# Kernel optimization log

Measured on AMD Instinct MI355X. Metric: run time of the kernel, lower is better.

## Reference

```python
import jax, jax.numpy as jnp
import numpy as np

EMBED_DIM = 1024
BLOCK = 2048
HEAD = 64
BATCH = 4


def setup_inputs() -> dict:
    key = jax.random.key(0)
    k0, k1, k2, k3 = jax.random.split(key, 4)
    tokens = jax.random.normal(k0, (BATCH, BLOCK, EMBED_DIM), dtype=jnp.float32)
    # torch Linear(embed_dim, head_size, bias=False): init ~ U(-1/sqrt(in), 1/sqrt(in)).
    s = 1.0 / np.sqrt(EMBED_DIM)
    Wq = jax.random.uniform(k1, (EMBED_DIM, HEAD), jnp.float32, -s, s)
    Wk = jax.random.uniform(k2, (EMBED_DIM, HEAD), jnp.float32, -s, s)
    Wv = jax.random.uniform(k3, (EMBED_DIM, HEAD), jnp.float32, -s, s)
    return {"tokens": tokens, "Wq": Wq, "Wk": Wk, "Wv": Wv}


def reference(tokens, Wq, Wk, Wv):
    B, S, E = tokens.shape
    q = jnp.einsum('bse,eh->bsh', tokens, Wq)
    k = jnp.einsum('bse,eh->bsh', tokens, Wk)
    v = jnp.einsum('bse,eh->bsh', tokens, Wv)
    # NOTE: module scales by embed_dim**-0.5 (not head_size).
    wei = jnp.einsum('bqh,bkh->bqk', q, k) * (E ** -0.5)
    causal = jnp.tril(jnp.ones((S, S), dtype=bool))  # tril_mask[:block,:block]
    wei = jnp.where(causal, wei, -1e9)
    wei = jax.nn.softmax(wei, axis=-1)
    # dropout(p=0.3) is identity in eval mode (deterministic reference)
    return jnp.einsum('bqk,bkh->bqh', wei, v)
```

## Files before the change

kernel.cpp:

```cpp
#include <hip/hip_runtime.h>
#include <stdint.h>


typedef __bf16 bf16_t;
typedef __bf16 bf16x8 __attribute__((ext_vector_type(8)));
typedef __bf16 bf16x4 __attribute__((ext_vector_type(4)));
typedef float floatx4 __attribute__((ext_vector_type(4)));

#define MFMA16(a, b, c) __builtin_amdgcn_mfma_f32_16x16x32_bf16((a), (b), (c), 0, 0, 0)

static constexpr float kQScale = 0.04508422002778f;
#define NEG_BIG (-3.0e38f)

__device__ inline bf16x4 cvt4(float4 f) {
  bf16x4 v;
  v[0] = (bf16_t)f.x; v[1] = (bf16_t)f.y; v[2] = (bf16_t)f.z; v[3] = (bf16_t)f.w;
  return v;
}

__global__ __launch_bounds__(256) void wt_kernel(const float* __restrict__ Wq,
                                                 const float* __restrict__ Wk,
                                                 const float* __restrict__ Wv,
                                                 bf16_t* __restrict__ Bp) {
  const int tid = blockIdx.x * 256 + threadIdx.x;
  const int j = tid & 7;
  const int lane = (tid >> 3) & 63;
  const int ks = (tid >> 9) & 31;
  const int nt = tid >> 14;
  const int m = nt >> 2, n4 = nt & 3;
  const int h = n4 * 16 + (lane & 15);
  const int e = ks * 32 + ((lane >> 4) << 3) + j;
  const float* W = (m == 0) ? Wq : ((m == 1) ? Wk : Wv);
  float v = W[e * 64 + h];
  if (m == 0) v *= kQScale;
  Bp[tid] = (bf16_t)v;
}

__global__ __launch_bounds__(256) void proj_kernel(const float* __restrict__ tok,
                                                   const bf16_t* __restrict__ Bp,
                                                   bf16_t* __restrict__ qw,
                                                   bf16_t* __restrict__ kw,
                                                   bf16_t* __restrict__ vw) {
  __shared__ bf16_t As[2][16][264];
  const int tx = threadIdx.x;
  const int wave = tx >> 6, lane = tx & 63;
  const int lanelo = lane & 15, quad = lane >> 4;
  const int grow = blockIdx.x * 16;
  const int b = grow >> 11;
  const int t = (grow & 2047) >> 4;

  const float* tokbase = tok + (grow + wave) * 1024 + lane * 4;

  floatx4 acc[3];
#pragma unroll
  for (int i = 0; i < 3; i++) acc[i] = (floatx4){0.f, 0.f, 0.f, 0.f};

  const bf16_t* bp[3];
#pragma unroll
  for (int j = 0; j < 3; j++)
    bp[j] = Bp + (wave * 3 + j) * 16384 + lane * 8;

  float4 tb[4];
#pragma unroll
  for (int r = 0; r < 4; r++) tb[r] = *(const float4*)(tokbase + r * 4096);
#pragma unroll
  for (int r = 0; r < 4; r++)
    *(bf16x4*)&As[0][r * 4 + wave][lane * 4] = cvt4(tb[r]);
  __syncthreads();

  for (int c = 0; c < 4; c++) {
    if (c < 3) {
#pragma unroll
      for (int r = 0; r < 4; r++)
        tb[r] = *(const float4*)(tokbase + r * 4096 + (c + 1) * 256);
    }
    const bf16_t* ab = &As[c & 1][lanelo][quad * 8];
#pragma unroll
    for (int ks = 0; ks < 8; ks++) {
      const bf16x8 af = *(const bf16x8*)(ab + ks * 32);
#pragma unroll
      for (int j = 0; j < 3; j++) {
        const bf16x8 bfr = *(const bf16x8*)(bp[j] + (c * 8 + ks) * 512);
        acc[j] = MFMA16(af, bfr, acc[j]);
      }
    }
    if (c < 3) {
#pragma unroll
      for (int r = 0; r < 4; r++)
        *(bf16x4*)&As[(c + 1) & 1][r * 4 + wave][lane * 4] = cvt4(tb[r]);
    }
    __syncthreads();
  }

  bf16_t* Cs = (bf16_t*)As;
#pragma unroll
  for (int j = 0; j < 3; j++) {
    const int nt = wave * 3 + j;
    const int n4 = nt & 3, mtx = nt >> 2;
    if (mtx < 2) {
#pragma unroll
      for (int r = 0; r < 4; r++)
        Cs[(quad * 4 + r) * 136 + mtx * 64 + n4 * 16 + lanelo] = (bf16_t)acc[j][r];
    } else {
      bf16x4 pk;
#pragma unroll
      for (int r = 0; r < 4; r++) pk[r] = (bf16_t)acc[j][r];
      const int base = (((b * 32 + (t >> 2)) * 2 + ((t >> 1) & 1)) * 4 + n4) * 512
                     + (quad * 16 + lanelo) * 8 + (t & 1) * 4;
      *(bf16x4*)(vw + base) = pk;
    }
  }
  __syncthreads();
  {
    const int mtx = tx >> 7, idx = tx & 127;
    const int ds = idx >> 6, lp = idx & 63;
    const int qr = lp & 15, h8 = ds * 32 + ((lp >> 4) << 3);
    const bf16x8 val = *(const bf16x8*)&Cs[qr * 136 + mtx * 64 + h8];
    bf16_t* dst = mtx ? kw : qw;
    *(bf16x8*)(dst + (b * 128 + t) * 1024 + idx * 8) = val;
  }
}

__global__ __launch_bounds__(512, 4) void attn_kernel(const bf16_t* __restrict__ qw,
                                                      const bf16_t* __restrict__ kw,
                                                      const bf16_t* __restrict__ vw,
                                                      float* __restrict__ out) {
  __shared__ float Ol[8][16][65];
  __shared__ float Ll[8][16];

  const int wave = threadIdx.x >> 6;
  const int lane = threadIdx.x & 63;
  const int lanelo = lane & 15;
  const int quad = lane >> 4;

  const int b = blockIdx.x & 3;
  const int t = 127 - (blockIdx.x >> 2);
  const int qbase = t * 16;
  const int grow = b * 2048 + qbase;

  const bf16_t* qp = qw + ((b * 128 + t) * 128 + lane) * 8;
  const bf16x8 qa0 = *(const bf16x8*)qp;
  const bf16x8 qa1 = *(const bf16x8*)(qp + 512);

  bf16x8 ones;
#pragma unroll
  for (int j = 0; j < 8; j++) ones[j] = (bf16_t)1.0f;

  floatx4 O[4];
#pragma unroll
  for (int i = 0; i < 4; i++) O[i] = (floatx4){0.f, 0.f, 0.f, 0.f};
  floatx4 lacc = (floatx4){0.f, 0.f, 0.f, 0.f};

  const int nch = (qbase + 16 + 63) >> 6;
  const bf16_t* kb = kw + b * 131072 + lane * 8;
  const bf16_t* vb = vw + b * 131072 + lane * 8;

  for (int c = wave; c < nch; c += 8) {
    const int cb = c * 64;
    floatx4 s[4];
    const floatx4 z = (floatx4){0.f, 0.f, 0.f, 0.f};
#pragma unroll
    for (int sub = 0; sub < 4; sub++) {
      const bf16_t* kp = kb + (c * 4 + sub) * 1024;
      s[sub] = MFMA16(*(const bf16x8*)kp, qa0, z);
      s[sub] = MFMA16(*(const bf16x8*)(kp + 512), qa1, s[sub]);
    }

    if (cb + 63 > qbase) {
#pragma unroll
      for (int sub = 0; sub < 4; sub++) {
        const int keyr = cb + sub * 16 + quad * 4;
#pragma unroll
        for (int r = 0; r < 4; r++)
          if (keyr + r > qbase + lanelo) s[sub][r] = NEG_BIG;
      }
    }

    bf16x8 pa0, pa1;
#pragma unroll
    for (int r = 0; r < 4; r++) {
      pa0[r]     = (bf16_t)__builtin_amdgcn_exp2f(s[0][r]);
      pa0[4 + r] = (bf16_t)__builtin_amdgcn_exp2f(s[1][r]);
      pa1[r]     = (bf16_t)__builtin_amdgcn_exp2f(s[2][r]);
      pa1[4 + r] = (bf16_t)__builtin_amdgcn_exp2f(s[3][r]);
    }

    const bf16_t* vp = vb + c * 4096;
#pragma unroll
    for (int dt = 0; dt < 4; dt++) {
      O[dt] = MFMA16(*(const bf16x8*)(vp + dt * 512), pa0, O[dt]);
      O[dt] = MFMA16(*(const bf16x8*)(vp + 2048 + dt * 512), pa1, O[dt]);
    }
    lacc = MFMA16(ones, pa0, lacc);
    lacc = MFMA16(ones, pa1, lacc);
  }

#pragma unroll
  for (int dt = 0; dt < 4; dt++)
#pragma unroll
    for (int r = 0; r < 4; r++)
      Ol[wave][lanelo][dt * 16 + quad * 4 + r] = O[dt][r];
  if (quad == 0) Ll[wave][lanelo] = lacc[0];
  __syncthreads();

#pragma unroll
  for (int o = threadIdx.x; o < 1024; o += 512) {
    const int row = o >> 6, d = o & 63;
    float L = 0.f, acc = 0.f;
#pragma unroll
    for (int w = 0; w < 8; w++) {
      L += Ll[w][row];
      acc += Ol[w][row][d];
    }
    out[(grow + row) * 64 + d] = acc / L;
  }
}

extern "C" void kernel_launch(void* const* d_in, const int* in_sizes, int n_in,
                              void* d_out, int out_size, void* d_ws, size_t ws_size,
                              hipStream_t stream) {
  const float* tokens = (const float*)d_in[0];
  const float* Wq = (const float*)d_in[1];
  const float* Wk = (const float*)d_in[2];
  const float* Wv = (const float*)d_in[3];
  float* out = (float*)d_out;

  char* ws = (char*)d_ws;
  if (ws_size < 3538944) return;
  bf16_t* Bp = (bf16_t*)ws;
  bf16_t* qw = (bf16_t*)(ws + 393216);
  bf16_t* kw = (bf16_t*)(ws + 393216 + 1048576);
  bf16_t* vw = (bf16_t*)(ws + 393216 + 2097152);

  hipLaunchKernelGGL(wt_kernel, dim3(768), dim3(256), 0, stream, Wq, Wk, Wv, Bp);
  hipLaunchKernelGGL(proj_kernel, dim3(512), dim3(256), 0, stream, tokens, Bp, qw, kw, vw);
  hipLaunchKernelGGL(attn_kernel, dim3(512), dim3(512), 0, stream, qw, kw, vw, out);
}
```

Baseline: 98.69 us.

## Fuse weight prep, projection, and attention into one cooperative persistent kernel

Replaces the three separate launches with a single cooperative kernel of 256 blocks that runs weight conversion, QKV projection and causal attention as phases separated by grid-wide syncs. Each block handles two tiles per phase, paired as i and 511-i, to balance the causal workload. The projection now stages a full 16x1024 token tile in shared memory and splits the K dimension across two wave groups, reducing their partial sums through shared memory. This removes launch gaps between kernels but adds grid-sync cost and runs only 256 blocks, which may lower occupancy. If the cooperative launch fails, it falls back to the old three kernels.

```diff
diff --git a/kernel.cpp b/kernel.cpp
--- a/kernel.cpp
+++ b/kernel.cpp
@@ -1,6 +1,9 @@
 #include <hip/hip_runtime.h>
+#include <hip/hip_cooperative_groups.h>
 #include <stdint.h>
 
+
+namespace cg = cooperative_groups;
 
 typedef __bf16 bf16_t;
 typedef __bf16 bf16x8 __attribute__((ext_vector_type(8)));
@@ -16,6 +19,215 @@
   bf16x4 v;
   v[0] = (bf16_t)f.x; v[1] = (bf16_t)f.y; v[2] = (bf16_t)f.z; v[3] = (bf16_t)f.w;
   return v;
+}
+
+#define SMEM_BYTES 33792
+
+__global__ __launch_bounds__(512, 4) void fused_kernel(
+    const float* __restrict__ tok, const float* __restrict__ Wq,
+    const float* __restrict__ Wk, const float* __restrict__ Wv,
+    bf16_t* __restrict__ Bp, bf16_t* __restrict__ qw,
+    bf16_t* __restrict__ kw, bf16_t* __restrict__ vw,
+    float* __restrict__ out) {
+  __shared__ __align__(16) char smem[SMEM_BYTES];
+  cg::grid_group gridg = cg::this_grid();
+
+  const int tx = threadIdx.x;
+  const int wave = tx >> 6, lane = tx & 63;
+  const int lanelo = lane & 15, quad = lane >> 4;
+
+#pragma unroll
+  for (int it = 0; it < 2; it++) {
+    const int tid = it * 131072 + blockIdx.x * 512 + tx;
+    if (tid < 196608) {
+      const int j = tid & 7;
+      const int ln = (tid >> 3) & 63;
+      const int ks = (tid >> 9) & 31;
+      const int nt = tid >> 14;
+      const int m = nt >> 2, n4 = nt & 3;
+      const int h = n4 * 16 + (ln & 15);
+      const int e = ks * 32 + ((ln >> 4) << 3) + j;
+      const float* W = (m == 0) ? Wq : ((m == 1) ? Wk : Wv);
+      float v = W[e * 64 + h];
+      if (m == 0) v *= kQScale;
+      Bp[tid] = (bf16_t)v;
+    }
+  }
+  __threadfence();
+  gridg.sync();
+  __threadfence();
+
+  for (int it = 0; it < 2; it++) {
+    __syncthreads();
+    const int tile = (it == 0) ? blockIdx.x : 511 - blockIdx.x;
+    bf16_t* As = (bf16_t*)smem;
+    const int grow = tile * 16;
+    const int b = grow >> 11;
+    const int t = (grow & 2047) >> 4;
+
+#pragma unroll
+    for (int i = 0; i < 8; i++) {
+      const int f = i * 512 + tx;
+      const int row = f >> 8, c4 = f & 255;
+      const float4 v = *(const float4*)(tok + (grow + row) * 1024 + c4 * 4);
+      *(bf16x4*)&As[row * 1032 + c4 * 4] = cvt4(v);
+    }
+    __syncthreads();
+
+    const int ng = wave & 3, kh = wave >> 2;
+    floatx4 acc[3];
+#pragma unroll
+    for (int i = 0; i < 3; i++) acc[i] = (floatx4){0.f, 0.f, 0.f, 0.f};
+    const bf16_t* bp[3];
+#pragma unroll
+    for (int j = 0; j < 3; j++)
+      bp[j] = Bp + (ng * 3 + j) * 16384 + lane * 8;
+    const bf16_t* ab = &As[lanelo * 1032 + quad * 8];
+
+#pragma unroll
+    for (int ks = 0; ks < 16; ks++) {
+      const int kk = kh * 16 + ks;
+      const bf16x8 af = *(const bf16x8*)(ab + kk * 32);
+#pragma unroll
+      for (int j = 0; j < 3; j++)
+        acc[j] = MFMA16(af, *(const bf16x8*)(bp[j] + kk * 512), acc[j]);
+    }
+    __syncthreads();
+
+    float* red = (float*)smem;
+    bf16_t* Cs = (bf16_t*)(smem + 12288);
+    if (kh == 1) {
+#pragma unroll
+      for (int j = 0; j < 3; j++)
+#pragma unroll
+        for (int r = 0; r < 4; r++)
+          red[(ng * 12 + j * 4 + r) * 64 + lane] = acc[j][r];
+    }
+    __syncthreads();
+    if (kh == 0) {
+#pragma unroll
+      for (int j = 0; j < 3; j++) {
+        const int nt = ng * 3 + j;
+        const int n4 = nt & 3, mtx = nt >> 2;
+#pragma unroll
+        for (int r = 0; r < 4; r++)
+          acc[j][r] += red[(ng * 12 + j * 4 + r) * 64 + lane];
+        if (mtx < 2) {
+#pragma unroll
+          for (int r = 0; r < 4; r++)
+            Cs[(quad * 4 + r) * 136 + mtx * 64 + n4 * 16 + lanelo] = (bf16_t)acc[j][r];
+        } else {
+          bf16x4 pk;
+#pragma unroll
+          for (int r = 0; r < 4; r++) pk[r] = (bf16_t)acc[j][r];
+          const int base = (((b * 32 + (t >> 2)) * 2 + ((t >> 1) & 1)) * 4 + n4) * 512
+                         + (quad * 16 + lanelo) * 8 + (t & 1) * 4;
+          *(bf16x4*)(vw + base) = pk;
+        }
+      }
+    }
+    __syncthreads();
+    if (tx < 256) {
+      const int mtx = tx >> 7, idx = tx & 127;
+      const int ds = idx >> 6, lp = idx & 63;
+      const int qr = lp & 15, h8 = ds * 32 + ((lp >> 4) << 3);
+      const bf16x8 val = *(const bf16x8*)&Cs[qr * 136 + mtx * 64 + h8];
+      bf16_t* dst = mtx ? kw : qw;
+      *(bf16x8*)(dst + (b * 128 + t) * 1024 + idx * 8) = val;
+    }
+  }
+  __threadfence();
+  gridg.sync();
+  __threadfence();
+
+  for (int it = 0; it < 2; it++) {
+    __syncthreads();
+    const int tile = (it == 0) ? blockIdx.x : 511 - blockIdx.x;
+    float* Ol = (float*)smem;
+    float* Ll = (float*)(smem + 33280);
+
+    const int b = tile & 3;
+    const int t = 127 - (tile >> 2);
+    const int qbase = t * 16;
+    const int grow = b * 2048 + qbase;
+
+    const bf16_t* qp = qw + ((b * 128 + t) * 128 + lane) * 8;
+    const bf16x8 qa0 = *(const bf16x8*)qp;
+    const bf16x8 qa1 = *(const bf16x8*)(qp + 512);
+
+    bf16x8 ones;
+#pragma unroll
+    for (int j = 0; j < 8; j++) ones[j] = (bf16_t)1.0f;
+
+    floatx4 O[4];
+#pragma unroll
+    for (int i = 0; i < 4; i++) O[i] = (floatx4){0.f, 0.f, 0.f, 0.f};
+    floatx4 lacc = (floatx4){0.f, 0.f, 0.f, 0.f};
+
+    const int nch = (qbase + 16 + 63) >> 6;
+    const bf16_t* kb = kw + b * 131072 + lane * 8;
+    const bf16_t* vb = vw + b * 131072 + lane * 8;
+
+    for (int c = wave; c < nch; c += 8) {
+      const int cb = c * 64;
+      floatx4 s[4];
+      const floatx4 z = (floatx4){0.f, 0.f, 0.f, 0.f};
+#pragma unroll
+      for (int sub = 0; sub < 4; sub++) {
+        const bf16_t* kp = kb + (c * 4 + sub) * 1024;
+        s[sub] = MFMA16(*(const bf16x8*)kp, qa0, z);
+        s[sub] = MFMA16(*(const bf16x8*)(kp + 512), qa1, s[sub]);
+      }
+
+      if (cb + 63 > qbase) {
+#pragma unroll
+        for (int sub = 0; sub < 4; sub++) {
+          const int keyr = cb + sub * 16 + quad * 4;
+#pragma unroll
+          for (int r = 0; r < 4; r++)
+            if (keyr + r > qbase + lanelo) s[sub][r] = NEG_BIG;
+        }
+      }
+
+      bf16x8 pa0, pa1;
+#pragma unroll
+      for (int r = 0; r < 4; r++) {
+        pa0[r]     = (bf16_t)__builtin_amdgcn_exp2f(s[0][r]);
+        pa0[4 + r] = (bf16_t)__builtin_amdgcn_exp2f(s[1][r]);
+        pa1[r]     = (bf16_t)__builtin_amdgcn_exp2f(s[2][r]);
+        pa1[4 + r] = (bf16_t)__builtin_amdgcn_exp2f(s[3][r]);
+      }
+
+      const bf16_t* vp = vb + c * 4096;
+#pragma unroll
+      for (int dt = 0; dt < 4; dt++) {
+        O[dt] = MFMA16(*(const bf16x8*)(vp + dt * 512), pa0, O[dt]);
+        O[dt] = MFMA16(*(const bf16x8*)(vp + 2048 + dt * 512), pa1, O[dt]);
+      }
+      lacc = MFMA16(ones, pa0, lacc);
+      lacc = MFMA16(ones, pa1, lacc);
+    }
+
+#pragma unroll
+    for (int dt = 0; dt < 4; dt++)
+#pragma unroll
+      for (int r = 0; r < 4; r++)
+        Ol[(wave * 16 + lanelo) * 65 + dt * 16 + quad * 4 + r] = O[dt][r];
+    if (quad == 0) Ll[wave * 16 + lanelo] = lacc[0];
+    __syncthreads();
+
+#pragma unroll
+    for (int o = tx; o < 1024; o += 512) {
+      const int row = o >> 6, d = o & 63;
+      float L = 0.f, acc = 0.f;
+#pragma unroll
+      for (int w = 0; w < 8; w++) {
+        L += Ll[w * 16 + row];
+        acc += Ol[(w * 16 + row) * 65 + d];
+      }
+      out[(grow + row) * 64 + d] = acc / L;
+    }
+  }
 }
 
 __global__ __launch_bounds__(256) void wt_kernel(const float* __restrict__ Wq,
@@ -232,7 +444,14 @@
   bf16_t* kw = (bf16_t*)(ws + 393216 + 1048576);
   bf16_t* vw = (bf16_t*)(ws + 393216 + 2097152);
 
-  hipLaunchKernelGGL(wt_kernel, dim3(768), dim3(256), 0, stream, Wq, Wk, Wv, Bp);
-  hipLaunchKernelGGL(proj_kernel, dim3(512), dim3(256), 0, stream, tokens, Bp, qw, kw, vw);
-  hipLaunchKernelGGL(attn_kernel, dim3(512), dim3(512), 0, stream, qw, kw, vw, out);
-}
+  void* args[] = {(void*)&tokens, (void*)&Wq, (void*)&Wk, (void*)&Wv,
+                  (void*)&Bp, (void*)&qw, (void*)&kw, (void*)&vw, (void*)&out};
+  hipError_t err = hipLaunchCooperativeKernel((const void*)fused_kernel,
+                                              dim3(256), dim3(512), args, 0,
+                                              stream);
+  if (err != hipSuccess) {
+    hipLaunchKernelGGL(wt_kernel, dim3(768), dim3(256), 0, stream, Wq, Wk, Wv, Bp);
+    hipLaunchKernelGGL(proj_kernel, dim3(512), dim3(256), 0, stream, tokens, Bp, qw, kw, vw);
+    hipLaunchKernelGGL(attn_kernel, dim3(512), dim3(512), 0, stream, qw, kw, vw, out);
+  }
+}
```

Measured after the change: 331.8 us. 236% more time.

## Process 32 token rows per projection block with 8 waves sharing weight tiles

Applied to the files above, without the earlier changes.

The projection kernel now handles 32 rows per block using 512 threads. Two groups of four waves each compute a 16-row half and read the same weight-fragment columns, so the block count halves from 512 to 256. The aim is to amortise weight loads and per-block overhead across more rows. The cost is fewer blocks in flight, which may underfill the 256 CUs, and larger shared memory per block.

```diff
diff --git a/kernel.cpp b/kernel.cpp
--- a/kernel.cpp
+++ b/kernel.cpp
@@ -36,20 +36,23 @@
   Bp[tid] = (bf16_t)v;
 }
 
-__global__ __launch_bounds__(256) void proj_kernel(const float* __restrict__ tok,
+__global__ __launch_bounds__(512) void proj_kernel(const float* __restrict__ tok,
                                                    const bf16_t* __restrict__ Bp,
                                                    bf16_t* __restrict__ qw,
                                                    bf16_t* __restrict__ kw,
                                                    bf16_t* __restrict__ vw) {
-  __shared__ bf16_t As[2][16][264];
+  __shared__ bf16_t As[2][32][264];
   const int tx = threadIdx.x;
   const int wave = tx >> 6, lane = tx & 63;
   const int lanelo = lane & 15, quad = lane >> 4;
-  const int grow = blockIdx.x * 16;
+  const int ng = wave & 3, rh = wave >> 2;
+  const int grow = blockIdx.x * 32;
   const int b = grow >> 11;
-  const int t = (grow & 2047) >> 4;
-
-  const float* tokbase = tok + (grow + wave) * 1024 + lane * 4;
+  const int t16 = ((grow & 2047) >> 4) + rh;
+
+  const int srow = tx >> 6;
+  const int sc4 = tx & 63;
+  const float* tokbase = tok + (grow + srow) * 1024 + sc4 * 4;
 
   floatx4 acc[3];
 #pragma unroll
@@ -58,23 +61,23 @@
   const bf16_t* bp[3];
 #pragma unroll
   for (int j = 0; j < 3; j++)
-    bp[j] = Bp + (wave * 3 + j) * 16384 + lane * 8;
+    bp[j] = Bp + (ng * 3 + j) * 16384 + lane * 8;
 
   float4 tb[4];
 #pragma unroll
-  for (int r = 0; r < 4; r++) tb[r] = *(const float4*)(tokbase + r * 4096);
-#pragma unroll
-  for (int r = 0; r < 4; r++)
-    *(bf16x4*)&As[0][r * 4 + wave][lane * 4] = cvt4(tb[r]);
+  for (int p = 0; p < 4; p++) tb[p] = *(const float4*)(tokbase + p * 8 * 1024);
+#pragma unroll
+  for (int p = 0; p < 4; p++)
+    *(bf16x4*)&As[0][srow + p * 8][sc4 * 4] = cvt4(tb[p]);
   __syncthreads();
 
   for (int c = 0; c < 4; c++) {
     if (c < 3) {
 #pragma unroll
-      for (int r = 0; r < 4; r++)
-        tb[r] = *(const float4*)(tokbase + r * 4096 + (c + 1) * 256);
-    }
-    const bf16_t* ab = &As[c & 1][lanelo][quad * 8];
+      for (int p = 0; p < 4; p++)
+        tb[p] = *(const float4*)(tokbase + p * 8 * 1024 + (c + 1) * 256);
+    }
+    const bf16_t* ab = &As[c & 1][rh * 16 + lanelo][quad * 8];
 #pragma unroll
     for (int ks = 0; ks < 8; ks++) {
       const bf16x8 af = *(const bf16x8*)(ab + ks * 32);
@@ -86,8 +89,8 @@
     }
     if (c < 3) {
 #pragma unroll
-      for (int r = 0; r < 4; r++)
-        *(bf16x4*)&As[(c + 1) & 1][r * 4 + wave][lane * 4] = cvt4(tb[r]);
+      for (int p = 0; p < 4; p++)
+        *(bf16x4*)&As[(c + 1) & 1][srow + p * 8][sc4 * 4] = cvt4(tb[p]);
     }
     __syncthreads();
   }
@@ -95,29 +98,33 @@
   bf16_t* Cs = (bf16_t*)As;
 #pragma unroll
   for (int j = 0; j < 3; j++) {
-    const int nt = wave * 3 + j;
+    const int nt = ng * 3 + j;
     const int n4 = nt & 3, mtx = nt >> 2;
     if (mtx < 2) {
 #pragma unroll
       for (int r = 0; r < 4; r++)
-        Cs[(quad * 4 + r) * 136 + mtx * 64 + n4 * 16 + lanelo] = (bf16_t)acc[j][r];
+        Cs[(rh * 16 + quad * 4 + r) * 136 + mtx * 64 + n4 * 16 + lanelo] =
+            (bf16_t)acc[j][r];
     } else {
       bf16x4 pk;
 #pragma unroll
       for (int r = 0; r < 4; r++) pk[r] = (bf16_t)acc[j][r];
-      const int base = (((b * 32 + (t >> 2)) * 2 + ((t >> 1) & 1)) * 4 + n4) * 512
-                     + (quad * 16 + lanelo) * 8 + (t & 1) * 4;
+      const int base = (((b * 32 + (t16 >> 2)) * 2 + ((t16 >> 1) & 1)) * 4 + n4) * 512
+                     + (quad * 16 + lanelo) * 8 + (t16 & 1) * 4;
       *(bf16x4*)(vw + base) = pk;
     }
   }
   __syncthreads();
   {
-    const int mtx = tx >> 7, idx = tx & 127;
+    const int rh2 = tx >> 8;
+    const int mtx = (tx >> 7) & 1;
+    const int idx = tx & 127;
     const int ds = idx >> 6, lp = idx & 63;
     const int qr = lp & 15, h8 = ds * 32 + ((lp >> 4) << 3);
-    const bf16x8 val = *(const bf16x8*)&Cs[qr * 136 + mtx * 64 + h8];
+    const bf16x8 val = *(const bf16x8*)&Cs[(rh2 * 16 + qr) * 136 + mtx * 64 + h8];
     bf16_t* dst = mtx ? kw : qw;
-    *(bf16x8*)(dst + (b * 128 + t) * 1024 + idx * 8) = val;
+    const int t2 = ((grow & 2047) >> 4) + rh2;
+    *(bf16x8*)(dst + (b * 128 + t2) * 1024 + idx * 8) = val;
   }
 }
 
@@ -233,6 +240,6 @@
   bf16_t* vw = (bf16_t*)(ws + 393216 + 2097152);
 
   hipLaunchKernelGGL(wt_kernel, dim3(768), dim3(256), 0, stream, Wq, Wk, Wv, Bp);
-  hipLaunchKernelGGL(proj_kernel, dim3(512), dim3(256), 0, stream, tokens, Bp, qw, kw, vw);
+  hipLaunchKernelGGL(proj_kernel, dim3(256), dim3(512), 0, stream, tokens, Bp, qw, kw, vw);
   hipLaunchKernelGGL(attn_kernel, dim3(512), dim3(512), 0, stream, qw, kw, vw, out);
 }
```

Result: slower. 101.4 us (+2.7%).
